# Optimization experiments

Hardware: AMD Instinct MI355X
Metric: run time of the kernel (lower is better)

The kernel has to match this reference:

```python
import jax, jax.numpy as jnp
import numpy as np

B, S, C = 4, 2048, 1024

def setup_inputs() -> dict:
    key = jax.random.key(0)
    ks = jax.random.split(key, 9)
    lim = 1.0 / np.sqrt(C)  # torch nn.Linear default init range
    def lin_params(kw, kb):
        W = jax.random.uniform(kw, (C, C), jnp.float32, -lim, lim)
        b = jax.random.uniform(kb, (C,), jnp.float32, -lim, lim)
        return W, b
    Wq, bq = lin_params(ks[0], ks[1])
    Wk, bk = lin_params(ks[2], ks[3])
    Wv, bv = lin_params(ks[4], ks[5])
    query = jax.random.normal(ks[6], (B, S, C), jnp.float32)
    key_t = jax.random.normal(ks[7], (B, S, C), jnp.float32)
    value = jax.random.normal(ks[8], (B, S, C), jnp.float32)
    return {"query": query, "key": key_t, "value": value,
            "Wq": Wq, "bq": bq, "Wk": Wk, "bk": bk, "Wv": Wv, "bv": bv}

def reference(query, key, value, Wq, bq, Wk, bk, Wv, bv):
    # Linear projections: y = x @ W^T + b (torch Linear convention, W is [out, in])
    Q = jnp.einsum('bsc,dc->bsd', query, Wq) + bq
    K = jnp.einsum('bsc,dc->bsd', key, Wk) + bk
    V = jnp.einsum('bsc,dc->bsd', value, Wv) + bv
    scale = jnp.float32(C) ** 0.5
    scores = jnp.einsum('bqd,bkd->bqk', Q, K) / scale  # [B, S, S]
    attn = jax.nn.softmax(scores, axis=-1)
    out = jnp.einsum('bqk,bkd->bqd', attn, V)  # [B, S, C]
    return out
```

## Files before the change

kernel.cpp:

```cpp
#include <hip/hip_runtime.h>
#include <hip/hip_bf16.h>


typedef _Float16 half8 __attribute__((ext_vector_type(8)));
typedef _Float16 half4 __attribute__((ext_vector_type(4)));
typedef float f32x4 __attribute__((ext_vector_type(4)));

#define AS1(p) ((const __attribute__((address_space(1))) void*)(p))
#define AS3(p) ((__attribute__((address_space(3))) void*)(p))

__global__ __launch_bounds__(256) void cvt3_f32_f16(
    const float* __restrict__ s0, const float* __restrict__ s1,
    const float* __restrict__ s2, _Float16* __restrict__ d0,
    _Float16* __restrict__ d1, _Float16* __restrict__ d2, int n) {
    const float* s = blockIdx.y == 0 ? s0 : blockIdx.y == 1 ? s1 : s2;
    _Float16* d = blockIdx.y == 0 ? d0 : blockIdx.y == 1 ? d1 : d2;
    int i = (blockIdx.x * 256 + threadIdx.x) * 8;
    if (i >= n) return;
    float4 a = *(const float4*)(s + i);
    float4 b = *(const float4*)(s + i + 4);
    half8 h;
    h[0] = (_Float16)a.x; h[1] = (_Float16)a.y; h[2] = (_Float16)a.z; h[3] = (_Float16)a.w;
    h[4] = (_Float16)b.x; h[5] = (_Float16)b.y; h[6] = (_Float16)b.z; h[7] = (_Float16)b.w;
    *(half8*)(d + i) = h;
}

template <int K, int TN, bool BIAS, bool F16OUT, bool TROUT, int GYS>
__global__ __launch_bounds__(256, 2)
void gemm_nt(const _Float16* __restrict__ A, const _Float16* __restrict__ Bt,
             const float* __restrict__ bias, void* __restrict__ Cout,
             int N, float scale, long sA, long sB, long sC) {
    constexpr int JN = TN / 32;
    constexpr int SLABS = (128 + TN) / 16;
    __shared__ _Float16 Asm[128 * 32] __attribute__((aligned(16)));
    __shared__ _Float16 Bsm[TN * 32] __attribute__((aligned(16)));
    const int tid = threadIdx.x;
    const int lane = tid & 63;
    const int wave = tid >> 6;

    const int lin = blockIdx.x;
    const int g = lin & 7;
    const int s = lin >> 3;
    const int xt = s & 15;
    const int row_id = g * 8 + (s >> 4);
    const int yt = row_id & ((1 << GYS) - 1);
    const long zb = row_id >> GYS;
    const int m0 = yt * 128;
    const int n0 = xt * TN;

    A += zb * sA;
    Bt += zb * sB;

    const int srow = lane >> 2;
    const int csw = (((lane & 3) ^ ((srow >> 1) & 3)) << 3);
    const int quad = lane >> 4;
    const int l16 = lane & 15;
    const int aswz = ((quad ^ ((l16 >> 1) & 3)) << 3);
    const int wm = (wave >> 1) << 6;
    const int wn = (wave & 1) * (TN >> 1);

    f32x4 acc[4][JN];
#pragma unroll
    for (int i = 0; i < 4; i++)
#pragma unroll
        for (int j = 0; j < JN; j++)
#pragma unroll
            for (int r = 0; r < 4; r++) acc[i][j][r] = 0.0f;

    const _Float16* Abase = A + (long)m0 * K;
    const _Float16* Bbase = Bt + (long)n0 * K;

    for (int k0 = 0; k0 < K; k0 += 32) {
        __syncthreads();
#pragma unroll
        for (int t = wave; t < SLABS; t += 4) {
            if (t < 8) {
                __builtin_amdgcn_global_load_lds(
                    AS1(Abase + (long)(t * 16 + srow) * K + k0 + csw),
                    AS3(Asm + t * 512), 16, 0, 0);
            } else {
                __builtin_amdgcn_global_load_lds(
                    AS1(Bbase + (long)((t - 8) * 16 + srow) * K + k0 + csw),
                    AS3(Bsm + (t - 8) * 512), 16, 0, 0);
            }
        }
        __syncthreads();

        half8 af[4], bf[JN];
#pragma unroll
        for (int i = 0; i < 4; i++)
            af[i] = *(const half8*)(Asm + (wm + i * 16 + l16) * 32 + aswz);
#pragma unroll
        for (int j = 0; j < JN; j++)
            bf[j] = *(const half8*)(Bsm + (wn + j * 16 + l16) * 32 + aswz);
#pragma unroll
        for (int i = 0; i < 4; i++)
#pragma unroll
            for (int j = 0; j < JN; j++)
                acc[i][j] = __builtin_amdgcn_mfma_f32_16x16x32_f16(af[i], bf[j], acc[i][j], 0, 0, 0);
    }

#pragma unroll
    for (int i = 0; i < 4; i++) {
        const int row = m0 + wm + i * 16 + quad * 4;
#pragma unroll
        for (int j = 0; j < JN; j++) {
            const int col = n0 + wn + j * 16 + l16;
            const float badd = BIAS ? bias[col] : 0.0f;
            if constexpr (TROUT) {
                const long b = row >> 11;
                const int sl = row & 2047;
                half4 h;
#pragma unroll
                for (int r = 0; r < 4; r++) h[r] = (_Float16)(acc[i][j][r] * scale + badd);
                *(half4*)((_Float16*)Cout + b * 2097152 + (long)col * 2048 + sl) = h;
            } else {
#pragma unroll
                for (int r = 0; r < 4; r++) {
                    float v = acc[i][j][r] * scale + badd;
                    if constexpr (F16OUT) {
                        ((_Float16*)Cout + zb * sC)[(long)(row + r) * N + col] = (_Float16)v;
                    } else {
                        ((float*)Cout + zb * sC)[(long)(row + r) * N + col] = v;
                    }
                }
            }
        }
    }
}

__global__ __launch_bounds__(256) void softmax_f16(const _Float16* __restrict__ S,
                                                   _Float16* __restrict__ P) {
    const long row = blockIdx.x;
    const int t = threadIdx.x;
    const int wave = t >> 6, lane = t & 63;
    half8 h = ((const half8*)(S + row * 2048))[t];
    float v[8];
#pragma unroll
    for (int j = 0; j < 8; j++) v[j] = (float)h[j];
    float m = v[0];
#pragma unroll
    for (int j = 1; j < 8; j++) m = fmaxf(m, v[j]);
#pragma unroll
    for (int off = 32; off > 0; off >>= 1) m = fmaxf(m, __shfl_xor(m, off, 64));
    __shared__ float redm[4], reds[4];
    if (lane == 0) redm[wave] = m;
    __syncthreads();
    m = fmaxf(fmaxf(redm[0], redm[1]), fmaxf(redm[2], redm[3]));
    float sum = 0.0f;
#pragma unroll
    for (int j = 0; j < 8; j++) { v[j] = __expf(v[j] - m); sum += v[j]; }
#pragma unroll
    for (int off = 32; off > 0; off >>= 1) sum += __shfl_xor(sum, off, 64);
    if (lane == 0) reds[wave] = sum;
    __syncthreads();
    sum = (reds[0] + reds[1]) + (reds[2] + reds[3]);
    const float inv = 1.0f / sum;
    half8 o;
#pragma unroll
    for (int j = 0; j < 8; j++) o[j] = (_Float16)(v[j] * inv);
    ((half8*)(P + row * 2048))[t] = o;
}

extern "C" void kernel_launch(void* const* d_in, const int* in_sizes, int n_in,
                              void* d_out, int out_size, void* d_ws, size_t ws_size,
                              hipStream_t stream) {
    constexpr int B = 4, S = 2048, C = 1024;
    constexpr long XSZ = (long)B * S * C;
    constexpr long WSZ = (long)C * C;

    const float* query = (const float*)d_in[0];
    const float* key   = (const float*)d_in[1];
    const float* value = (const float*)d_in[2];
    const float* Wq = (const float*)d_in[3];
    const float* bq = (const float*)d_in[4];
    const float* Wk = (const float*)d_in[5];
    const float* bk = (const float*)d_in[6];
    const float* Wv = (const float*)d_in[7];
    const float* bv = (const float*)d_in[8];
    float* out = (float*)d_out;
    char* ws = (char*)d_ws;

    _Float16* Xq  = (_Float16*)(ws + 0);
    _Float16* Xk  = (_Float16*)(ws + XSZ * 2);
    _Float16* Xv  = (_Float16*)(ws + 2 * XSZ * 2);
    _Float16* Wqh = (_Float16*)(ws + 3 * XSZ * 2);
    _Float16* Wkh = (_Float16*)(ws + 3 * XSZ * 2 + WSZ * 2);
    _Float16* Wvh = (_Float16*)(ws + 3 * XSZ * 2 + 2 * WSZ * 2);
    _Float16* scores = (_Float16*)(ws + 0);
    _Float16* Qh  = (_Float16*)(ws + 73400320);
    _Float16* Kh  = (_Float16*)(ws + 73400320 + XSZ * 2);
    _Float16* attn = (_Float16*)(ws + 73400320);
    _Float16* Vt  = (_Float16*)(ws + 106954752);
    if (ws_size < 123731968) return;

    cvt3_f32_f16<<<dim3(XSZ / 2048, 3), 256, 0, stream>>>(query, key, value, Xq, Xk, Xv, (int)XSZ);
    cvt3_f32_f16<<<dim3(WSZ / 2048, 3), 256, 0, stream>>>(Wq, Wk, Wv, Wqh, Wkh, Wvh, (int)WSZ);

    gemm_nt<1024, 64, true, true, false, 6><<<1024, 256, 0, stream>>>(Xq, Wqh, bq, Qh, C, 1.0f, 0, 0, 0);
    gemm_nt<1024, 64, true, true, false, 6><<<1024, 256, 0, stream>>>(Xk, Wkh, bk, Kh, C, 1.0f, 0, 0, 0);
    gemm_nt<1024, 64, true, true, true, 6><<<1024, 256, 0, stream>>>(Xv, Wvh, bv, Vt, C, 1.0f, 0, 0, 0);

    gemm_nt<1024, 128, false, true, false, 4><<<1024, 256, 0, stream>>>(
        Qh, Kh, nullptr, scores, S, 0.03125f, (long)S * C, (long)S * C, (long)S * S);

    softmax_f16<<<B * S, 256, 0, stream>>>(scores, attn);

    gemm_nt<2048, 64, false, false, false, 4><<<1024, 256, 0, stream>>>(
        attn, Vt, nullptr, out, C, 1.0f, (long)S * S, (long)C * S, (long)S * C);
}
```

Baseline: 353.7 us.

## Use 128x128x64 GEMM tiles and merge QKV projections into one launch

The GEMM kernel now always uses 128x128 output tiles with a 64-wide K step and a new XOR swizzle, which halves the barrier count per K and raises data reuse per LDS load. The three Q/K/V projection GEMMs are fused into one 1536-block launch that picks bias and output (transposed for V) per z-tile. The PV GEMM now launches 512 larger blocks. The cost is 32KB of LDS per block and more accumulator registers, which may lower occupancy, and the PV grid of 512 blocks may underfill the GPU.

```diff
diff --git a/kernel.cpp b/kernel.cpp
--- a/kernel.cpp
+++ b/kernel.cpp
@@ -25,15 +25,15 @@
     *(half8*)(d + i) = h;
 }
 
-template <int K, int TN, bool BIAS, bool F16OUT, bool TROUT, int GYS>
+template <int K, int NX_SH, int R, int NYT_SH, bool BIAS, bool F16OUT, bool PROJ3>
 __global__ __launch_bounds__(256, 2)
 void gemm_nt(const _Float16* __restrict__ A, const _Float16* __restrict__ Bt,
-             const float* __restrict__ bias, void* __restrict__ Cout,
-             int N, float scale, long sA, long sB, long sC) {
-    constexpr int JN = TN / 32;
-    constexpr int SLABS = (128 + TN) / 16;
-    __shared__ _Float16 Asm[128 * 32] __attribute__((aligned(16)));
-    __shared__ _Float16 Bsm[TN * 32] __attribute__((aligned(16)));
+             const float* __restrict__ b0, const float* __restrict__ b1,
+             const float* __restrict__ b2, void* __restrict__ Cout,
+             _Float16* __restrict__ VtOut, int N, float scale,
+             long sA, long sB, long sC) {
+    __shared__ _Float16 Asm[128 * 64] __attribute__((aligned(16)));
+    __shared__ _Float16 Bsm[128 * 64] __attribute__((aligned(16)));
     const int tid = threadIdx.x;
     const int lane = tid & 63;
     const int wave = tid >> 6;
@@ -41,88 +41,107 @@
     const int lin = blockIdx.x;
     const int g = lin & 7;
     const int s = lin >> 3;
-    const int xt = s & 15;
-    const int row_id = g * 8 + (s >> 4);
-    const int yt = row_id & ((1 << GYS) - 1);
-    const long zb = row_id >> GYS;
+    const int xt = s & ((1 << NX_SH) - 1);
+    const int row_id = g * R + (s >> NX_SH);
+    const int yt = row_id & ((1 << NYT_SH) - 1);
+    const int tz = row_id >> NYT_SH;
     const int m0 = yt * 128;
-    const int n0 = xt * TN;
-
-    A += zb * sA;
-    Bt += zb * sB;
-
-    const int srow = lane >> 2;
-    const int csw = (((lane & 3) ^ ((srow >> 1) & 3)) << 3);
+    const int n0 = xt * 128;
+
+    const float* bias = nullptr;
+    if constexpr (PROJ3) {
+        A += (long)tz * 8388608;
+        Bt += (long)tz * 1048576;
+        bias = tz == 0 ? b0 : tz == 1 ? b1 : b2;
+    } else {
+        A += (long)tz * sA;
+        Bt += (long)tz * sB;
+    }
+
+    const int srow8 = lane >> 3;
+    const int sq = ((lane & 7) ^ srow8) << 3;
     const int quad = lane >> 4;
     const int l16 = lane & 15;
-    const int aswz = ((quad ^ ((l16 >> 1) & 3)) << 3);
     const int wm = (wave >> 1) << 6;
-    const int wn = (wave & 1) * (TN >> 1);
-
-    f32x4 acc[4][JN];
+    const int wn = (wave & 1) << 6;
+    const int fa0 = (wm + l16) * 64 + (((0 * 4 + quad) ^ (l16 & 7)) << 3);
+    const int fa1 = (wm + l16) * 64 + (((1 * 4 + quad) ^ (l16 & 7)) << 3);
+    const int fb0 = (wn + l16) * 64 + (((0 * 4 + quad) ^ (l16 & 7)) << 3);
+    const int fb1 = (wn + l16) * 64 + (((1 * 4 + quad) ^ (l16 & 7)) << 3);
+
+    f32x4 acc[4][4];
 #pragma unroll
     for (int i = 0; i < 4; i++)
 #pragma unroll
-        for (int j = 0; j < JN; j++)
+        for (int j = 0; j < 4; j++)
 #pragma unroll
             for (int r = 0; r < 4; r++) acc[i][j][r] = 0.0f;
 
     const _Float16* Abase = A + (long)m0 * K;
     const _Float16* Bbase = Bt + (long)n0 * K;
 
-    for (int k0 = 0; k0 < K; k0 += 32) {
+    for (int k0 = 0; k0 < K; k0 += 64) {
         __syncthreads();
 #pragma unroll
-        for (int t = wave; t < SLABS; t += 4) {
-            if (t < 8) {
+        for (int u = 0; u < 8; ++u) {
+            const int t = wave + u * 4;
+            if (t < 16) {
                 __builtin_amdgcn_global_load_lds(
-                    AS1(Abase + (long)(t * 16 + srow) * K + k0 + csw),
+                    AS1(Abase + (long)(t * 8 + srow8) * K + k0 + sq),
                     AS3(Asm + t * 512), 16, 0, 0);
             } else {
                 __builtin_amdgcn_global_load_lds(
-                    AS1(Bbase + (long)((t - 8) * 16 + srow) * K + k0 + csw),
-                    AS3(Bsm + (t - 8) * 512), 16, 0, 0);
+                    AS1(Bbase + (long)((t - 16) * 8 + srow8) * K + k0 + sq),
+                    AS3(Bsm + (t - 16) * 512), 16, 0, 0);
             }
         }
         __syncthreads();
 
-        half8 af[4], bf[JN];
-#pragma unroll
-        for (int i = 0; i < 4; i++)
-            af[i] = *(const half8*)(Asm + (wm + i * 16 + l16) * 32 + aswz);
-#pragma unroll
-        for (int j = 0; j < JN; j++)
-            bf[j] = *(const half8*)(Bsm + (wn + j * 16 + l16) * 32 + aswz);
-#pragma unroll
-        for (int i = 0; i < 4; i++)
-#pragma unroll
-            for (int j = 0; j < JN; j++)
-                acc[i][j] = __builtin_amdgcn_mfma_f32_16x16x32_f16(af[i], bf[j], acc[i][j], 0, 0, 0);
+#pragma unroll
+        for (int ks = 0; ks < 2; ++ks) {
+            const int ao = ks ? fa1 : fa0;
+            const int bo = ks ? fb1 : fb0;
+            half8 af[4], bf[4];
+#pragma unroll
+            for (int i = 0; i < 4; i++) af[i] = *(const half8*)(Asm + ao + i * 1024);
+#pragma unroll
+            for (int j = 0; j < 4; j++) bf[j] = *(const half8*)(Bsm + bo + j * 1024);
+#pragma unroll
+            for (int i = 0; i < 4; i++)
+#pragma unroll
+                for (int j = 0; j < 4; j++)
+                    acc[i][j] = __builtin_amdgcn_mfma_f32_16x16x32_f16(af[i], bf[j], acc[i][j], 0, 0, 0);
+        }
     }
 
+    const bool trout = PROJ3 && tz == 2;
 #pragma unroll
     for (int i = 0; i < 4; i++) {
         const int row = m0 + wm + i * 16 + quad * 4;
 #pragma unroll
-        for (int j = 0; j < JN; j++) {
+        for (int j = 0; j < 4; j++) {
             const int col = n0 + wn + j * 16 + l16;
             const float badd = BIAS ? bias[col] : 0.0f;
-            if constexpr (TROUT) {
+            if (trout) {
                 const long b = row >> 11;
                 const int sl = row & 2047;
                 half4 h;
 #pragma unroll
                 for (int r = 0; r < 4; r++) h[r] = (_Float16)(acc[i][j][r] * scale + badd);
-                *(half4*)((_Float16*)Cout + b * 2097152 + (long)col * 2048 + sl) = h;
+                *(half4*)(VtOut + b * 2097152 + (long)col * 2048 + sl) = h;
+            } else if constexpr (PROJ3) {
+                _Float16* o = (_Float16*)Cout + (long)tz * 8388608;
+#pragma unroll
+                for (int r = 0; r < 4; r++)
+                    o[(long)(row + r) * N + col] = (_Float16)(acc[i][j][r] * scale + badd);
             } else {
 #pragma unroll
                 for (int r = 0; r < 4; r++) {
                     float v = acc[i][j][r] * scale + badd;
-                    if constexpr (F16OUT) {
-                        ((_Float16*)Cout + zb * sC)[(long)(row + r) * N + col] = (_Float16)v;
-                    } else {
-                        ((float*)Cout + zb * sC)[(long)(row + r) * N + col] = v;
-                    }
+                    if constexpr (F16OUT)
+                        ((_Float16*)Cout + (long)tz * sC)[(long)(row + r) * N + col] = (_Float16)v;
+                    else
+                        ((float*)Cout + (long)tz * sC)[(long)(row + r) * N + col] = v;
                 }
             }
         }
@@ -182,30 +201,28 @@
     char* ws = (char*)d_ws;
 
     _Float16* Xq  = (_Float16*)(ws + 0);
-    _Float16* Xk  = (_Float16*)(ws + XSZ * 2);
-    _Float16* Xv  = (_Float16*)(ws + 2 * XSZ * 2);
     _Float16* Wqh = (_Float16*)(ws + 3 * XSZ * 2);
-    _Float16* Wkh = (_Float16*)(ws + 3 * XSZ * 2 + WSZ * 2);
-    _Float16* Wvh = (_Float16*)(ws + 3 * XSZ * 2 + 2 * WSZ * 2);
     _Float16* scores = (_Float16*)(ws + 0);
     _Float16* Qh  = (_Float16*)(ws + 73400320);
-    _Float16* Kh  = (_Float16*)(ws + 73400320 + XSZ * 2);
     _Float16* attn = (_Float16*)(ws + 73400320);
     _Float16* Vt  = (_Float16*)(ws + 106954752);
     if (ws_size < 123731968) return;
 
-    cvt3_f32_f16<<<dim3(XSZ / 2048, 3), 256, 0, stream>>>(query, key, value, Xq, Xk, Xv, (int)XSZ);
-    cvt3_f32_f16<<<dim3(WSZ / 2048, 3), 256, 0, stream>>>(Wq, Wk, Wv, Wqh, Wkh, Wvh, (int)WSZ);
-
-    gemm_nt<1024, 64, true, true, false, 6><<<1024, 256, 0, stream>>>(Xq, Wqh, bq, Qh, C, 1.0f, 0, 0, 0);
-    gemm_nt<1024, 64, true, true, false, 6><<<1024, 256, 0, stream>>>(Xk, Wkh, bk, Kh, C, 1.0f, 0, 0, 0);
-    gemm_nt<1024, 64, true, true, true, 6><<<1024, 256, 0, stream>>>(Xv, Wvh, bv, Vt, C, 1.0f, 0, 0, 0);
-
-    gemm_nt<1024, 128, false, true, false, 4><<<1024, 256, 0, stream>>>(
-        Qh, Kh, nullptr, scores, S, 0.03125f, (long)S * C, (long)S * C, (long)S * S);
+    cvt3_f32_f16<<<dim3(XSZ / 2048, 3), 256, 0, stream>>>(
+        query, key, value, Xq, Xq + XSZ, Xq + 2 * XSZ, (int)XSZ);
+    cvt3_f32_f16<<<dim3(WSZ / 2048, 3), 256, 0, stream>>>(
+        Wq, Wk, Wv, Wqh, Wqh + WSZ, Wqh + 2 * WSZ, (int)WSZ);
+
+    gemm_nt<1024, 3, 24, 6, true, true, true><<<1536, 256, 0, stream>>>(
+        Xq, Wqh, bq, bk, bv, Qh, Vt, C, 1.0f, 0, 0, 0);
+
+    gemm_nt<1024, 4, 8, 4, false, true, false><<<1024, 256, 0, stream>>>(
+        Qh, Qh + XSZ, nullptr, nullptr, nullptr, scores, nullptr, S, 0.03125f,
+        (long)S * C, (long)S * C, (long)S * S);
 
     softmax_f16<<<B * S, 256, 0, stream>>>(scores, attn);
 
-    gemm_nt<2048, 64, false, false, false, 4><<<1024, 256, 0, stream>>>(
-        attn, Vt, nullptr, out, C, 1.0f, (long)S * S, (long)C * S, (long)S * C);
-}
+    gemm_nt<2048, 3, 8, 4, false, false, false><<<512, 256, 0, stream>>>(
+        attn, Vt, nullptr, nullptr, nullptr, out, nullptr, C, 1.0f,
+        (long)S * S, (long)C * S, (long)S * C);
+}
```

Result: faster. 308.2 us (-12.9%).
